# Kernel tuning notes

Measured on AMD Instinct MI355X. Metric: run time of the kernel, lower is better.

## Reference

```python
import jax, jax.numpy as jnp
import numpy as np

HIDDEN = 1024
N_HEADS = 16
N_KV_HEADS = 4
HEAD_DIM = HIDDEN // N_HEADS  # 64
GROUPS = N_HEADS // N_KV_HEADS  # 4


def setup_inputs() -> dict:
    key = jax.random.key(0)
    k1, k2, k3, k4 = jax.random.split(key, 4)
    B, T = 2, 2048
    s = 0.02
    x = jax.random.normal(k1, (B, T, HIDDEN), dtype=jnp.float32)
    Wq = jax.random.normal(k2, (HIDDEN, N_HEADS * HEAD_DIM), dtype=jnp.float32) * s
    Wkv = jax.random.normal(k3, (HIDDEN, 2 * N_KV_HEADS * HEAD_DIM), dtype=jnp.float32) * s
    Wo = jax.random.normal(k4, (N_HEADS * HEAD_DIM, HIDDEN), dtype=jnp.float32) * s
    return {"x": x, "Wq": Wq, "Wkv": Wkv, "Wo": Wo}


def reference(x, Wq, Wkv, Wo):
    B, T, _ = x.shape
    scale = HEAD_DIM ** -0.5
    q = (x @ Wq).reshape(B, T, N_HEADS, HEAD_DIM).transpose(0, 2, 1, 3)  # [B,H,T,D]
    kv = x @ Wkv
    k, v = jnp.split(kv, 2, axis=-1)
    k = k.reshape(B, T, N_KV_HEADS, HEAD_DIM).transpose(0, 2, 1, 3)  # [B,Hkv,T,D]
    v = v.reshape(B, T, N_KV_HEADS, HEAD_DIM).transpose(0, 2, 1, 3)
    # repeat_interleave over head dim -> [B,H,T,D]
    k = jnp.repeat(k, GROUPS, axis=1)
    v = jnp.repeat(v, GROUPS, axis=1)
    scores = jnp.einsum("bhqd,bhkd->bhqk", q, k) * scale
    causal = jnp.triu(jnp.ones((T, T), dtype=bool), k=1)
    scores = jnp.where(causal[None, None], -jnp.inf, scores)
    w = jax.nn.softmax(scores, axis=-1)
    out = jnp.einsum("bhqk,bhkd->bhqd", w, v)
    out = out.transpose(0, 2, 1, 3).reshape(B, T, N_HEADS * HEAD_DIM)
    return out @ Wo
```

## Files before the change

kernel.cpp:

```cpp
#include <hip/hip_runtime.h>

using bf16x8 = __attribute__((ext_vector_type(8))) __bf16;
using f32x4  = __attribute__((ext_vector_type(4))) float;

__device__ __forceinline__ short f2bf(float f) {
  unsigned u = __builtin_bit_cast(unsigned, f);
  u += 0x7fffu + ((u >> 16) & 1u);
  return (short)(u >> 16);
}

__device__ __forceinline__ void gll16(const void* g, void* l) {
  __builtin_amdgcn_global_load_lds((const __attribute__((address_space(1))) unsigned*)g,
                                   (__attribute__((address_space(3))) unsigned*)l, 16, 0, 0);
}

__global__ void convert_bf16(const float* __restrict__ in, short* __restrict__ out, int n) {
  int i = (blockIdx.x * blockDim.x + threadIdx.x) * 4;
  if (i + 3 < n) {
    float4 f = *(const float4*)(&in[i]);
    short4 o;
    o.x = f2bf(f.x); o.y = f2bf(f.y); o.z = f2bf(f.z); o.w = f2bf(f.w);
    *(short4*)(&out[i]) = o;
  }
}

__global__ void prep_weights(const float* __restrict__ Wq, const float* __restrict__ Wkv,
                             const float* __restrict__ Wo,
                             short* __restrict__ Wqkvt, short* __restrict__ Wot) {
  __shared__ short tile[32][33];
  const int z = blockIdx.z;
  const float* src; short* dst; int C;
  if (z == 0)      { src = Wq;  dst = Wqkvt;               C = 1024; }
  else if (z == 1) { if (blockIdx.x >= 16) return;
                     src = Wkv; dst = Wqkvt + 1024 * 1024; C = 512;  }
  else             { src = Wo;  dst = Wot;                 C = 1024; }
  int c0 = blockIdx.x * 32, r0 = blockIdx.y * 32;
  for (int i = threadIdx.y; i < 32; i += 8)
    tile[i][threadIdx.x] = f2bf(src[(r0 + i) * C + c0 + threadIdx.x]);
  __syncthreads();
  for (int i = threadIdx.y; i < 32; i += 8)
    dst[(c0 + i) * 1024L + r0 + threadIdx.x] = tile[threadIdx.x][i];
}

__global__ void transpose_v(const short* __restrict__ QKV, short* __restrict__ Vt) {
  __shared__ short tile[32][33];
  int tt = blockIdx.x, dt = blockIdx.y, bkv = blockIdx.z;
  int b = bkv >> 2, kvh = bkv & 3;
  int t0 = tt * 32, d0 = dt * 32;
  for (int i = threadIdx.y; i < 32; i += 8)
    tile[i][threadIdx.x] = QKV[((long)(b * 2048 + t0 + i)) * 1536 + 1280 + kvh * 64 + d0 + threadIdx.x];
  __syncthreads();
  for (int i = threadIdx.y; i < 32; i += 8)
    Vt[((long)(bkv * 64 + d0 + i)) * 2048 + t0 + threadIdx.x] = tile[threadIdx.x][i];
}

template <bool OUT_BF16>
__global__ __launch_bounds__(256) void gemm_bt(const short* __restrict__ A,
                                               const short* __restrict__ Bt,
                                               void* __restrict__ Cout,
                                               int N, int K) {
  __shared__ __attribute__((aligned(16))) short sA[2][64 * 64];
  __shared__ __attribute__((aligned(16))) short sB[2][128 * 64];
  const int tid  = threadIdx.x;
  const int bm   = blockIdx.y * 64, bn = blockIdx.x * 128;
  const int wave = tid >> 6, lane = tid & 63;
  const int wm = (wave >> 1) * 32, wn = (wave & 1) * 64;
  const int qd = lane >> 4, c16 = lane & 15;

  f32x4 acc[2][4] = {};

  auto stage = [&](int it, int d) {
    int k0 = it * 64;
#pragma unroll
    for (int i = 0; i < 2; i++) {
      int c = i * 256 + tid;
      int r = c >> 3, cc = c & 7;
      gll16(&A[(bm + r) * (long)K + k0 + ((cc ^ (r & 7)) * 8)],
            &sA[d][(i * 256 + wave * 64) * 8]);
    }
#pragma unroll
    for (int i = 0; i < 4; i++) {
      int c = i * 256 + tid;
      int r = c >> 3, cc = c & 7;
      gll16(&Bt[(bn + r) * (long)K + k0 + ((cc ^ (r & 7)) * 8)],
            &sB[d][(i * 256 + wave * 64) * 8]);
    }
  };

  const int niter = K >> 6;
  stage(0, 0);
  for (int it = 0; it < niter; it++) {
    const int cur = it & 1;
    asm volatile("" ::: "memory");
    __builtin_amdgcn_s_barrier();
    if (it + 1 < niter) {
      stage(it + 1, cur ^ 1);
      asm volatile("s_waitcnt vmcnt(6)" ::: "memory");
    } else {
      asm volatile("s_waitcnt vmcnt(0)" ::: "memory");
    }
    __builtin_amdgcn_s_barrier();
    asm volatile("" ::: "memory");

    bf16x8 af[2][2], bfr[4][2];
#pragma unroll
    for (int mt = 0; mt < 2; mt++) {
      int rr = wm + mt * 16 + c16;
#pragma unroll
      for (int ks = 0; ks < 2; ks++)
        af[mt][ks] = *(const bf16x8*)(&sA[cur][rr * 64 + (((ks * 4 + qd) ^ (rr & 7)) * 8)]);
    }
#pragma unroll
    for (int nt = 0; nt < 4; nt++) {
      int rr = wn + nt * 16 + c16;
#pragma unroll
      for (int ks = 0; ks < 2; ks++)
        bfr[nt][ks] = *(const bf16x8*)(&sB[cur][rr * 64 + (((ks * 4 + qd) ^ (rr & 7)) * 8)]);
    }
#pragma unroll
    for (int ks = 0; ks < 2; ks++)
#pragma unroll
      for (int mt = 0; mt < 2; mt++)
#pragma unroll
        for (int nt = 0; nt < 4; nt++)
          acc[mt][nt] = __builtin_amdgcn_mfma_f32_16x16x32_bf16(af[mt][ks], bfr[nt][ks],
                                                                acc[mt][nt], 0, 0, 0);
  }

#pragma unroll
  for (int mt = 0; mt < 2; mt++)
#pragma unroll
    for (int nt = 0; nt < 4; nt++)
#pragma unroll
      for (int r = 0; r < 4; r++) {
        long row = bm + wm + mt * 16 + qd * 4 + r;
        long col = bn + wn + nt * 16 + c16;
        float v = acc[mt][nt][r];
        if constexpr (OUT_BF16) ((short*)Cout)[row * N + col] = f2bf(v);
        else                    ((float*)Cout)[row * N + col] = v;
      }
}

#define CSOFT 0.18033688f
#define CMAX  (CSOFT * 12.0f)

__global__ __launch_bounds__(256) void attn_kernel(const short* __restrict__ QKV,
                                                   const short* __restrict__ Vt,
                                                   short* __restrict__ Aout) {
  const int bx = blockIdx.x;
  const int qt = (bx < 512) ? (127 - (bx >> 3)) : ((bx >> 3) - 64);
  const int kvh = (bx >> 1) & 3, b = bx & 1;
  const int bkv = b * 4 + kvh;
  const int tid = threadIdx.x;
  const int w = tid >> 6, lane = tid & 63;
  const int qd = lane >> 4, c16 = lane & 15;
  const int h = kvh * 4 + w;
  const int q0 = qt * 16;

  __shared__ __attribute__((aligned(16))) short sK[2][64 * 64];
  __shared__ __attribute__((aligned(16))) short sVt[2][64 * 64];
  __shared__ __attribute__((aligned(16))) short sP[4][16 * 72];

  auto stage = [&](int kt, int d) {
#pragma unroll
    for (int i = 0; i < 2; i++) {
      int c = i * 256 + tid;
      int r = c >> 3, cc = c & 7;
      gll16(&QKV[((long)(b * 2048 + kt * 64 + r)) * 1536 + 1024 + kvh * 64 + ((cc ^ (r & 7)) * 8)],
            &sK[d][(i * 256 + w * 64) * 8]);
      gll16(&Vt[((long)(bkv * 64 + r)) * 2048 + kt * 64 + ((cc ^ (r & 7)) * 8)],
            &sVt[d][(i * 256 + w * 64) * 8]);
    }
  };

  stage(0, 0);

  bf16x8 qf[2];
  {
    long tok = (long)b * 2048 + q0 + c16;
#pragma unroll
    for (int ks = 0; ks < 2; ks++)
      qf[ks] = *(const bf16x8*)(&QKV[tok * 1536 + h * 64 + ks * 32 + qd * 8]);
  }

  f32x4 Ot[4] = {};
  float l_i = 0.f;

  const int ntiles = (qt >> 2) + 1;
  for (int kt = 0; kt < ntiles; kt++) {
    const int cur = kt & 1;
    asm volatile("" ::: "memory");
    __builtin_amdgcn_s_barrier();
    if (kt + 1 < ntiles) {
      stage(kt + 1, cur ^ 1);
      asm volatile("s_waitcnt vmcnt(4)" ::: "memory");
    } else {
      asm volatile("s_waitcnt vmcnt(0)" ::: "memory");
    }
    __builtin_amdgcn_s_barrier();
    asm volatile("" ::: "memory");

    f32x4 St[4];
#pragma unroll
    for (int jc = 0; jc < 4; jc++) {
      int rr = jc * 16 + c16;
      bf16x8 kf0 = *(const bf16x8*)(&sK[cur][rr * 64 + ((0 + qd) ^ (rr & 7)) * 8]);
      bf16x8 kf1 = *(const bf16x8*)(&sK[cur][rr * 64 + ((4 + qd) ^ (rr & 7)) * 8]);
      f32x4 z = {};
      z = __builtin_amdgcn_mfma_f32_16x16x32_bf16(kf0, qf[0], z, 0, 0, 0);
      z = __builtin_amdgcn_mfma_f32_16x16x32_bf16(kf1, qf[1], z, 0, 0, 0);
      St[jc] = z;
    }

    if (kt == ntiles - 1) {
      int qg = q0 + c16 - kt * 64;
#pragma unroll
      for (int jc = 0; jc < 4; jc++)
#pragma unroll
        for (int r = 0; r < 4; r++)
          if (jc * 16 + qd * 4 + r > qg) St[jc][r] = -3e38f;
    }

    {
      float rs = 0.f;
#pragma unroll
      for (int jc = 0; jc < 4; jc++) {
        unsigned u[4];
#pragma unroll
        for (int r = 0; r < 4; r++) {
          float p = exp2f(fmaf(CSOFT, St[jc][r], -CMAX));
          u[r] = __builtin_bit_cast(unsigned, p) & 0xffff0000u;
          rs += __builtin_bit_cast(float, u[r]);
        }
        int2 pk;
        pk.x = (int)((u[0] >> 16) | u[1]);
        pk.y = (int)((u[2] >> 16) | u[3]);
        *(int2*)(&sP[w][c16 * 72 + jc * 16 + qd * 4]) = pk;
      }
      l_i += rs;
    }
    asm volatile("s_waitcnt lgkmcnt(0)" ::: "memory");

#pragma unroll
    for (int ks2 = 0; ks2 < 2; ks2++) {
      bf16x8 pf = *(const bf16x8*)(&sP[w][c16 * 72 + ks2 * 32 + qd * 8]);
#pragma unroll
      for (int dt = 0; dt < 4; dt++) {
        int rr = dt * 16 + c16;
        bf16x8 vf = *(const bf16x8*)(&sVt[cur][rr * 64 + (((ks2 * 4 + qd) ^ (rr & 7)) * 8)]);
        Ot[dt] = __builtin_amdgcn_mfma_f32_16x16x32_bf16(vf, pf, Ot[dt], 0, 0, 0);
      }
    }
  }

  {
    float l = l_i;
    l += __shfl_xor(l, 16, 64);
    l += __shfl_xor(l, 32, 64);
    float inv = 1.f / l;
    long tok = (long)b * 2048 + q0 + c16;
#pragma unroll
    for (int dt = 0; dt < 4; dt++) {
      short4 o;
      o.x = f2bf(Ot[dt][0] * inv);
      o.y = f2bf(Ot[dt][1] * inv);
      o.z = f2bf(Ot[dt][2] * inv);
      o.w = f2bf(Ot[dt][3] * inv);
      *(short4*)(&Aout[tok * 1024 + h * 64 + dt * 16 + qd * 4]) = o;
    }
  }
}

extern "C" void kernel_launch(void* const* d_in, const int* in_sizes, int n_in,
                              void* d_out, int out_size, void* d_ws, size_t ws_size,
                              hipStream_t stream) {
  const float* x   = (const float*)d_in[0];
  const float* Wq  = (const float*)d_in[1];
  const float* Wkv = (const float*)d_in[2];
  const float* Wo  = (const float*)d_in[3];

  char* ws = (char*)d_ws;
  short* xb    = (short*)(ws);
  short* Wqkvt = (short*)(ws + 8388608);
  short* Wot   = (short*)(ws + 11534336);
  short* QKV   = (short*)(ws + 13631488);
  short* attn  = (short*)(ws + 26214400);
  short* Vtb   = (short*)(ws);

  convert_bf16<<<4096, 256, 0, stream>>>(x, xb, 4194304);
  prep_weights<<<dim3(32, 32, 3), dim3(32, 8), 0, stream>>>(Wq, Wkv, Wo, Wqkvt, Wot);

  gemm_bt<true><<<dim3(12, 64), 256, 0, stream>>>(xb, Wqkvt, QKV, 1536, 1024);
  transpose_v<<<dim3(64, 2, 8), dim3(32, 8), 0, stream>>>(QKV, Vtb);
  attn_kernel<<<dim3(1024), 256, 0, stream>>>(QKV, Vtb, attn);
  gemm_bt<false><<<dim3(8, 64), 256, 0, stream>>>(attn, Wot, d_out, 1024, 1024);
}
```

Baseline: 164.0 us.

## Fuse prep kernels, write V transpose from QKV GEMM epilogue, single-buffer V in attention

Merges the x conversion and weight transposes into one launch. The QKV GEMM epilogue now writes transposed V directly into the output buffer, which serves as scratch, so the separate transpose kernel goes away. Attention single-buffers V in shared memory, loading each tile in the same iteration behind an extra barrier, and adds an occupancy hint of 4 blocks. This removes two launches and one pass over V, in exchange for extra scattered short4 stores in the GEMM epilogue and less overlap of V loads with compute.

```diff
diff --git a/kernel.cpp b/kernel.cpp
--- a/kernel.cpp
+++ b/kernel.cpp
@@ -14,50 +14,42 @@
                                    (__attribute__((address_space(3))) unsigned*)l, 16, 0, 0);
 }
 
-__global__ void convert_bf16(const float* __restrict__ in, short* __restrict__ out, int n) {
-  int i = (blockIdx.x * blockDim.x + threadIdx.x) * 4;
-  if (i + 3 < n) {
-    float4 f = *(const float4*)(&in[i]);
+__global__ __launch_bounds__(256) void fused_pre(const float* __restrict__ x,
+                                                 const float* __restrict__ Wq,
+                                                 const float* __restrict__ Wkv,
+                                                 const float* __restrict__ Wo,
+                                                 short* __restrict__ xb,
+                                                 short* __restrict__ Wqkvt,
+                                                 short* __restrict__ Wot) {
+  const int bx = blockIdx.x, tid = threadIdx.x;
+  if (bx < 4096) {
+    int i = (bx * 256 + tid) * 4;
+    float4 f = *(const float4*)(&x[i]);
     short4 o;
     o.x = f2bf(f.x); o.y = f2bf(f.y); o.z = f2bf(f.z); o.w = f2bf(f.w);
-    *(short4*)(&out[i]) = o;
-  }
-}
-
-__global__ void prep_weights(const float* __restrict__ Wq, const float* __restrict__ Wkv,
-                             const float* __restrict__ Wo,
-                             short* __restrict__ Wqkvt, short* __restrict__ Wot) {
+    *(short4*)(&xb[i]) = o;
+    return;
+  }
   __shared__ short tile[32][33];
-  const int z = blockIdx.z;
-  const float* src; short* dst; int C;
-  if (z == 0)      { src = Wq;  dst = Wqkvt;               C = 1024; }
-  else if (z == 1) { if (blockIdx.x >= 16) return;
-                     src = Wkv; dst = Wqkvt + 1024 * 1024; C = 512;  }
-  else             { src = Wo;  dst = Wot;                 C = 1024; }
-  int c0 = blockIdx.x * 32, r0 = blockIdx.y * 32;
-  for (int i = threadIdx.y; i < 32; i += 8)
-    tile[i][threadIdx.x] = f2bf(src[(r0 + i) * C + c0 + threadIdx.x]);
+  const float* src; short* dst; int C, ti;
+  if (bx < 5120)      { src = Wq;  dst = Wqkvt;               C = 1024; ti = bx - 4096; }
+  else if (bx < 5632) { src = Wkv; dst = Wqkvt + 1024 * 1024; C = 512;  ti = bx - 5120; }
+  else                { src = Wo;  dst = Wot;                 C = 1024; ti = bx - 5632; }
+  int ctiles = C >> 5;
+  int c0 = (ti % ctiles) * 32, r0 = (ti / ctiles) * 32;
+  int tx = tid & 31, ty = tid >> 5;
+  for (int i = ty; i < 32; i += 8)
+    tile[i][tx] = f2bf(src[(r0 + i) * C + c0 + tx]);
   __syncthreads();
-  for (int i = threadIdx.y; i < 32; i += 8)
-    dst[(c0 + i) * 1024L + r0 + threadIdx.x] = tile[threadIdx.x][i];
-}
-
-__global__ void transpose_v(const short* __restrict__ QKV, short* __restrict__ Vt) {
-  __shared__ short tile[32][33];
-  int tt = blockIdx.x, dt = blockIdx.y, bkv = blockIdx.z;
-  int b = bkv >> 2, kvh = bkv & 3;
-  int t0 = tt * 32, d0 = dt * 32;
-  for (int i = threadIdx.y; i < 32; i += 8)
-    tile[i][threadIdx.x] = QKV[((long)(b * 2048 + t0 + i)) * 1536 + 1280 + kvh * 64 + d0 + threadIdx.x];
-  __syncthreads();
-  for (int i = threadIdx.y; i < 32; i += 8)
-    Vt[((long)(bkv * 64 + d0 + i)) * 2048 + t0 + threadIdx.x] = tile[threadIdx.x][i];
-}
-
-template <bool OUT_BF16>
+  for (int i = ty; i < 32; i += 8)
+    dst[(c0 + i) * 1024L + r0 + tx] = tile[tx][i];
+}
+
+template <bool OUT_BF16, bool WRITE_VT>
 __global__ __launch_bounds__(256) void gemm_bt(const short* __restrict__ A,
                                                const short* __restrict__ Bt,
                                                void* __restrict__ Cout,
+                                               short* __restrict__ Vt,
                                                int N, int K) {
   __shared__ __attribute__((aligned(16))) short sA[2][64 * 64];
   __shared__ __attribute__((aligned(16))) short sB[2][128 * 64];
@@ -130,23 +122,34 @@
 #pragma unroll
   for (int mt = 0; mt < 2; mt++)
 #pragma unroll
-    for (int nt = 0; nt < 4; nt++)
+    for (int nt = 0; nt < 4; nt++) {
+      long row0 = bm + wm + mt * 16 + qd * 4;
+      long col  = bn + wn + nt * 16 + c16;
+      short4 p;
 #pragma unroll
       for (int r = 0; r < 4; r++) {
-        long row = bm + wm + mt * 16 + qd * 4 + r;
-        long col = bn + wn + nt * 16 + c16;
         float v = acc[mt][nt][r];
-        if constexpr (OUT_BF16) ((short*)Cout)[row * N + col] = f2bf(v);
-        else                    ((float*)Cout)[row * N + col] = v;
+        if constexpr (OUT_BF16) ((short*)Cout)[(row0 + r) * N + col] = f2bf(v);
+        else                    ((float*)Cout)[(row0 + r) * N + col] = v;
+        if constexpr (WRITE_VT)
+          ((short*)&p)[r] = f2bf(v);
       }
+      if constexpr (WRITE_VT) {
+        if (col >= 1280) {
+          int d = (int)col - 1280;
+          int b = (int)(row0 >> 11), t = (int)(row0 & 2047);
+          *(short4*)(&Vt[((long)(b * 256 + d)) * 2048 + t]) = p;
+        }
+      }
+    }
 }
 
 #define CSOFT 0.18033688f
 #define CMAX  (CSOFT * 12.0f)
 
-__global__ __launch_bounds__(256) void attn_kernel(const short* __restrict__ QKV,
-                                                   const short* __restrict__ Vt,
-                                                   short* __restrict__ Aout) {
+__global__ __launch_bounds__(256, 4) void attn_kernel(const short* __restrict__ QKV,
+                                                      const short* __restrict__ Vt,
+                                                      short* __restrict__ Aout) {
   const int bx = blockIdx.x;
   const int qt = (bx < 512) ? (127 - (bx >> 3)) : ((bx >> 3) - 64);
   const int kvh = (bx >> 1) & 3, b = bx & 1;
@@ -158,22 +161,29 @@
   const int q0 = qt * 16;
 
   __shared__ __attribute__((aligned(16))) short sK[2][64 * 64];
-  __shared__ __attribute__((aligned(16))) short sVt[2][64 * 64];
+  __shared__ __attribute__((aligned(16))) short sVt[64 * 64];
   __shared__ __attribute__((aligned(16))) short sP[4][16 * 72];
 
-  auto stage = [&](int kt, int d) {
+  auto stageK = [&](int kt, int d) {
 #pragma unroll
     for (int i = 0; i < 2; i++) {
       int c = i * 256 + tid;
       int r = c >> 3, cc = c & 7;
       gll16(&QKV[((long)(b * 2048 + kt * 64 + r)) * 1536 + 1024 + kvh * 64 + ((cc ^ (r & 7)) * 8)],
             &sK[d][(i * 256 + w * 64) * 8]);
+    }
+  };
+  auto stageV = [&](int kt) {
+#pragma unroll
+    for (int i = 0; i < 2; i++) {
+      int c = i * 256 + tid;
+      int r = c >> 3, cc = c & 7;
       gll16(&Vt[((long)(bkv * 64 + r)) * 2048 + kt * 64 + ((cc ^ (r & 7)) * 8)],
-            &sVt[d][(i * 256 + w * 64) * 8]);
+            &sVt[(i * 256 + w * 64) * 8]);
     }
   };
 
-  stage(0, 0);
+  stageK(0, 0);
 
   bf16x8 qf[2];
   {
@@ -191,11 +201,12 @@
     const int cur = kt & 1;
     asm volatile("" ::: "memory");
     __builtin_amdgcn_s_barrier();
+    stageV(kt);
     if (kt + 1 < ntiles) {
-      stage(kt + 1, cur ^ 1);
+      stageK(kt + 1, cur ^ 1);
       asm volatile("s_waitcnt vmcnt(4)" ::: "memory");
     } else {
-      asm volatile("s_waitcnt vmcnt(0)" ::: "memory");
+      asm volatile("s_waitcnt vmcnt(2)" ::: "memory");
     }
     __builtin_amdgcn_s_barrier();
     asm volatile("" ::: "memory");
@@ -241,13 +252,18 @@
     }
     asm volatile("s_waitcnt lgkmcnt(0)" ::: "memory");
 
+    if (kt + 1 < ntiles) asm volatile("s_waitcnt vmcnt(2)" ::: "memory");
+    else                 asm volatile("s_waitcnt vmcnt(0)" ::: "memory");
+    __builtin_amdgcn_s_barrier();
+    asm volatile("" ::: "memory");
+
 #pragma unroll
     for (int ks2 = 0; ks2 < 2; ks2++) {
       bf16x8 pf = *(const bf16x8*)(&sP[w][c16 * 72 + ks2 * 32 + qd * 8]);
 #pragma unroll
       for (int dt = 0; dt < 4; dt++) {
         int rr = dt * 16 + c16;
-        bf16x8 vf = *(const bf16x8*)(&sVt[cur][rr * 64 + (((ks2 * 4 + qd) ^ (rr & 7)) * 8)]);
+        bf16x8 vf = *(const bf16x8*)(&sVt[rr * 64 + (((ks2 * 4 + qd) ^ (rr & 7)) * 8)]);
         Ot[dt] = __builtin_amdgcn_mfma_f32_16x16x32_bf16(vf, pf, Ot[dt], 0, 0, 0);
       }
     }
@@ -285,13 +301,13 @@
   short* Wot   = (short*)(ws + 11534336);
   short* QKV   = (short*)(ws + 13631488);
   short* attn  = (short*)(ws + 26214400);
-  short* Vtb   = (short*)(ws);
-
-  convert_bf16<<<4096, 256, 0, stream>>>(x, xb, 4194304);
-  prep_weights<<<dim3(32, 32, 3), dim3(32, 8), 0, stream>>>(Wq, Wkv, Wo, Wqkvt, Wot);
-
-  gemm_bt<true><<<dim3(12, 64), 256, 0, stream>>>(xb, Wqkvt, QKV, 1536, 1024);
-  transpose_v<<<dim3(64, 2, 8), dim3(32, 8), 0, stream>>>(QKV, Vtb);
+  short* Vtb   = (short*)d_out;
+
+  fused_pre<<<dim3(6656), 256, 0, stream>>>(x, Wq, Wkv, Wo, xb, Wqkvt, Wot);
+
+  gemm_bt<true, true><<<dim3(12, 64), 256, 0, stream>>>(xb, Wqkvt, QKV, Vtb, 1536, 1024);
+
   attn_kernel<<<dim3(1024), 256, 0, stream>>>(QKV, Vtb, attn);
-  gemm_bt<false><<<dim3(8, 64), 256, 0, stream>>>(attn, Wot, d_out, 1024, 1024);
-}
+
+  gemm_bt<false, false><<<dim3(8, 64), 256, 0, stream>>>(attn, Wot, d_out, nullptr, 1024, 1024);
+}
```

Measured after the change: 157.4 us. 4.0% less time.
